# Kernel optimization log

Measured on AMD Instinct MI355X. Metric: run time of the kernel, lower is better.

## Reference

```python
import jax, jax.numpy as jnp
import numpy as np

CASCADING_LOSS = 0.85


def _bilinear_sample(img, px, py):
    """grid_sample(align_corners=True, padding_mode='zeros') in pixel coords.
    img: [B,C,H,W]; px,py: [B,H,W] absolute pixel coordinates."""
    B, C, H, W = img.shape
    x0 = jnp.floor(px)
    y0 = jnp.floor(py)
    x1 = x0 + 1.0
    y1 = y0 + 1.0
    wx1 = px - x0
    wx0 = 1.0 - wx1
    wy1 = py - y0
    wy0 = 1.0 - wy1

    def gather(yi, xi):
        valid = (xi >= 0) & (xi <= W - 1) & (yi >= 0) & (yi <= H - 1)
        xc = jnp.clip(xi, 0, W - 1).astype(jnp.int32)
        yc = jnp.clip(yi, 0, H - 1).astype(jnp.int32)
        # per-batch advanced indexing: [B,C,H,W]
        vals = jax.vmap(lambda im, yy, xx: im[:, yy, xx])(img, yc, xc)
        return vals * valid[:, None, :, :].astype(img.dtype)

    out = (gather(y0, x0) * (wy0 * wx0)[:, None, :, :]
           + gather(y0, x1) * (wy0 * wx1)[:, None, :, :]
           + gather(y1, x0) * (wy1 * wx0)[:, None, :, :]
           + gather(y1, x1) * (wy1 * wx1)[:, None, :, :])
    return out


def _add_flow(img, flw):
    # img: [B,C,H,W]; flw: [B,2,H,W] with channel 0 -> y offset, channel 1 -> x offset
    B, C, H, W = img.shape
    base_x = jnp.arange(W, dtype=img.dtype)[None, None, :]   # [1,1,W]
    base_y = jnp.arange(H, dtype=img.dtype)[None, :, None]   # [1,H,1]
    px = base_x + flw[:, 1, :, :]
    py = base_y + flw[:, 0, :, :]
    return _bilinear_sample(img, px, py)


def _compute_psnr(target, estim):
    mse = jnp.mean((target - estim) ** 2)
    return 10.0 * jnp.log(1.0 / mse) / jnp.log(jnp.asarray(10.0, target.dtype))


def setup_inputs() -> dict:
    key = jax.random.key(0)
    k1, k2, k3 = jax.random.split(key, 3)
    ITERS, B, H, W, C = 12, 4, 384, 512, 3
    flow_tup = jax.random.normal(k1, (ITERS, B, 2, H, W), dtype=jnp.float32)
    frame1 = jax.random.uniform(k2, (B, C, H, W), dtype=jnp.float32)
    frame2 = jax.random.uniform(k3, (B, C, H, W), dtype=jnp.float32)
    return {"flow_tup": flow_tup, "frame1": frame1, "frame2": frame2}


def reference(flow_tup, frame1, frame2):
    n_iters = flow_tup.shape[0]
    # vectorize warp over GRU iterations
    estims = jax.vmap(lambda f: _add_flow(frame1, f))(flow_tup)  # [I,B,C,H,W]
    psnrs = jax.vmap(lambda e: _compute_psnr(frame2, e))(estims)  # [I]
    weights = CASCADING_LOSS ** (n_iters - jnp.arange(n_iters, dtype=flow_tup.dtype))
    loss = -jnp.sum(psnrs * weights)
    return loss
```

## Files before the change

kernel.cpp:

```cpp
#include <hip/hip_runtime.h>
#include <math.h>

typedef _Float16 h2 __attribute__((ext_vector_type(2)));

static __device__ __forceinline__ h2 pkrtz(float a, float b) {
    return __builtin_bit_cast(h2, __builtin_amdgcn_cvt_pkrtz(a, b));
}

#if defined(__has_builtin)
#  if __has_builtin(__builtin_amdgcn_fdot2)
#    define HAVE_FDOT2 1
#  endif
#endif

#define ITERS 12
#define BATCH 4
#define CH 3
#define H 384
#define W 512

constexpr int HW  = H * W;
constexpr int CHW = CH * HW;
constexpr int TILE_X = 32, TILE_Y = 16;
constexpr int TX_N = W / TILE_X;
constexpr int TY_N = H / TILE_Y;
constexpr int NBLK = BATCH * TX_N * TY_N;
constexpr int HALO = 8;
constexpr int WIN_W = TILE_X + 2 * HALO;
constexpr int WROW  = WIN_W + 1;
constexpr int WIN_H = TILE_Y + 2 * HALO;
constexpr int WIN_CELLS = WROW * WIN_H;
constexpr int FSTRIDE = BATCH * 2 * HW;
constexpr int NXCD = 8;
constexpr int CHUNK = NBLK / NXCD;

__global__ __launch_bounds__(256, 6) void warp_mse_kernel(
    const float* __restrict__ flow,
    const float* __restrict__ f1,
    const float* __restrict__ f2,
    float* __restrict__ partials)
{
    __shared__ uint2 win[WIN_CELLS];

    int tid = threadIdx.x;
    int bx0 = blockIdx.x;
    int bx  = (bx0 & (NXCD - 1)) * CHUNK + (bx0 >> 3);
    int b   = bx / (TX_N * TY_N);
    int t   = bx - b * (TX_N * TY_N);
    int ty  = t / TX_N;
    int tx  = t - ty * TX_N;
    int x_t = tx * TILE_X, y_t = ty * TILE_Y;

    const float* f1b = f1 + b * CHW;
    const float* f2b = f2 + b * CHW;

    int x = x_t + 2 * (tid & 15);
    int y = y_t + (tid >> 4);
    int p = y * W + x;
    float yf = (float)y;
    const int ABASE = -((y_t - HALO) * WROW + (x_t - HALO));

    float2 tc0 = *(const float2*)(f2b + p);
    float2 tc1 = *(const float2*)(f2b + HW + p);
    float2 tc2 = *(const float2*)(f2b + 2 * HW + p);
    const float* fp = flow + b * 2 * HW + p;
    float2 fy0 = *(const float2*)(fp);
    float2 fx0 = *(const float2*)(fp + HW);
    float2 fy1 = *(const float2*)(fp + FSTRIDE);
    float2 fx1 = *(const float2*)(fp + FSTRIDE + HW);

#pragma unroll
    for (int k = 0; k < 3; ++k) {
        int q   = tid + 256 * k;
        int row = q / (WIN_W / 2);
        int cp  = q - row * (WIN_W / 2);
        int gx0 = x_t - HALO + 2 * cp;
        int gy  = y_t - HALO + row;
        int gxc = min(max(gx0, 0), W - 2);
        int gyc = min(max(gy, 0), H - 1);
        const float* src = f1b + gyc * W + gxc;
        float2 c0 = *(const float2*)(src);
        float2 c1 = *(const float2*)(src + HW);
        float2 c2 = *(const float2*)(src + 2 * HW);
        bool vy = (unsigned)gy < (unsigned)H;
        bool v0 = vy && ((unsigned)gx0 < (unsigned)W);
        bool v1 = vy && ((unsigned)(gx0 + 1) < (unsigned)W);
        if (!v0) { c0.x = 0.0f; c1.x = 0.0f; c2.x = 0.0f; }
        if (!v1) { c0.y = 0.0f; c1.y = 0.0f; c2.y = 0.0f; }
        unsigned a0 = __builtin_bit_cast(unsigned, pkrtz(c0.x, c1.x));
        unsigned b0 = __builtin_bit_cast(unsigned, pkrtz(c2.x, 0.0f));
        unsigned a1 = __builtin_bit_cast(unsigned, pkrtz(c0.y, c1.y));
        unsigned b1 = __builtin_bit_cast(unsigned, pkrtz(c2.y, 0.0f));
        int wb = row * WROW + 2 * cp;
        win[wb]     = make_uint2(a0, b0);
        win[wb + 1] = make_uint2(a1, b1);
    }
    __syncthreads();

    h2 t01[2], t2p[2];
    t01[0] = pkrtz(tc0.x, tc1.x);
    t2p[0] = pkrtz(tc2.x, 0.0f);
    t01[1] = pkrtz(tc0.y, tc1.y);
    t2p[1] = pkrtz(tc2.y, 0.0f);

    alignas(16) float acc[ITERS];
#pragma unroll
    for (int k = 0; k < ITERS; ++k) acc[k] = 0.0f;

#pragma unroll
    for (int it = 0; it < ITERS; ++it) {
        const float* fp2 = fp + 2 * FSTRIDE;
        float2 fy2 = make_float2(0.0f, 0.0f), fx2 = make_float2(0.0f, 0.0f);
        if (it + 2 < ITERS) { fy2 = *(const float2*)(fp2); fx2 = *(const float2*)(fp2 + HW); }

        float a_it = 0.0f;
#pragma unroll
        for (int j = 0; j < 2; ++j) {
            float fy = j ? fy0.y : fy0.x;
            float fx = j ? fx0.y : fx0.x;
            float pxf = (float)(x + j) + fx;
            float pyf = yf + fy;
            float x0f = floorf(pxf), y0f = floorf(pyf);
            float wx1 = pxf - x0f, wy1 = pyf - y0f;

            int a = (int)y0f * WROW + (int)x0f + ABASE;
            a = min(max(a, 0), WIN_CELLS - WROW - 2);

            uint2 c00 = win[a];
            uint2 c10 = win[a + WROW];
            uint2 c01 = win[a + 1];
            uint2 c11 = win[a + WROW + 1];

            h2 wxh = pkrtz(wx1, wx1);
            h2 wyh = pkrtz(wy1, wy1);

            h2 p00 = __builtin_bit_cast(h2, c00.x);
            h2 p01 = __builtin_bit_cast(h2, c01.x);
            h2 p10 = __builtin_bit_cast(h2, c10.x);
            h2 p11 = __builtin_bit_cast(h2, c11.x);
            h2 q00 = __builtin_bit_cast(h2, c00.y);
            h2 q01 = __builtin_bit_cast(h2, c01.y);
            h2 q10 = __builtin_bit_cast(h2, c10.y);
            h2 q11 = __builtin_bit_cast(h2, c11.y);

            h2 tA = p00 + (p01 - p00) * wxh;
            h2 bA = p10 + (p11 - p10) * wxh;
            h2 v01 = tA + (bA - tA) * wyh;
            h2 tB = q00 + (q01 - q00) * wxh;
            h2 bB = q10 + (q11 - q10) * wxh;
            h2 v2  = tB + (bB - tB) * wyh;

            h2 d01 = t01[j] - v01;
            h2 d2  = t2p[j] - v2;
#ifdef HAVE_FDOT2
            a_it = __builtin_amdgcn_fdot2(d01, d01,
                     __builtin_amdgcn_fdot2(d2, d2, a_it, false), false);
#else
            a_it += (float)d01.x * (float)d01.x + (float)d01.y * (float)d01.y
                  + (float)d2.x * (float)d2.x;
#endif
        }
        acc[it] = a_it;
        fy0 = fy1; fx0 = fx1; fy1 = fy2; fx1 = fx2; fp += FSTRIDE;
    }

    __syncthreads();
    float* scr = (float*)win;
    float4* sc4 = (float4*)scr;
    const float4* av = (const float4*)acc;
    sc4[tid * 3 + 0] = av[0];
    sc4[tid * 3 + 1] = av[1];
    sc4[tid * 3 + 2] = av[2];
    __syncthreads();

    int lane = tid & 63;
    int wv   = tid >> 6;
#pragma unroll
    for (int r = 0; r < 3; ++r) {
        int k = wv + 4 * r;
        float s = scr[lane * 12 + k]
                + scr[(lane + 64) * 12 + k]
                + scr[(lane + 128) * 12 + k]
                + scr[(lane + 192) * 12 + k];
#pragma unroll
        for (int off = 32; off > 0; off >>= 1)
            s += __shfl_down(s, off, 64);
        if (lane == 0) partials[k * NBLK + bx] = s;
    }
}

__global__ __launch_bounds__(768) void finalize_kernel(
    const float* __restrict__ partials,
    float* __restrict__ out)
{
    __shared__ float psnr_w[ITERS];
    int wave = threadIdx.x >> 6;
    int lane = threadIdx.x & 63;

    float s = 0.0f;
    const float4* pp = (const float4*)(partials + wave * NBLK);
#pragma unroll
    for (int j = 0; j < NBLK / 256; ++j) {
        float4 v = pp[lane + 64 * j];
        s += (v.x + v.y) + (v.z + v.w);
    }
#pragma unroll
    for (int off = 32; off > 0; off >>= 1)
        s += __shfl_down(s, off, 64);

    if (lane == 0) {
        float mse  = s * (1.0f / (float)(BATCH * CH * HW));
        float psnr = -10.0f * 0.30102999566398f * log2f(mse);
        float w = 1.0f;
        for (int k = 0; k < ITERS - wave; ++k) w *= 0.85f;
        psnr_w[wave] = psnr * w;
    }
    __syncthreads();
    if (threadIdx.x == 0) {
        float loss = 0.0f;
#pragma unroll
        for (int i = 0; i < ITERS; ++i) loss += psnr_w[i];
        out[0] = -loss;
    }
}

extern "C" void kernel_launch(void* const* d_in, const int* in_sizes, int n_in,
                              void* d_out, int out_size, void* d_ws, size_t ws_size,
                              hipStream_t stream) {
    const float* flow = (const float*)d_in[0];
    const float* f1   = (const float*)d_in[1];
    const float* f2   = (const float*)d_in[2];
    float* out        = (float*)d_out;
    float* partials   = (float*)d_ws;

    warp_mse_kernel<<<NBLK, 256, 0, stream>>>(flow, f1, f2, partials);
    finalize_kernel<<<1, 768, 0, stream>>>(partials, out);
}
```

Before: 127.3 us.

## Load flow as float4 per lane pair and exchange halves via shuffles

Each adjacent lane pair now loads four flow values as one float4 per lane: even lanes read the y-offset plane and odd lanes read the x-offset plane. The two lanes swap halves with __shfl_xor, so each still gets its own fy/fx pair. This replaces two float2 loads per iteration with one wider load, and the prefetch depth grows from two iterations ahead to three. The cost is extra cross-lane shuffles and selects, plus higher register pressure from the deeper float4 prefetch queue.

```diff
diff --git a/kernel.cpp b/kernel.cpp
--- a/kernel.cpp
+++ b/kernel.cpp
@@ -30,6 +30,7 @@
 constexpr int WROW  = WIN_W + 1;
 constexpr int WIN_H = TILE_Y + 2 * HALO;
 constexpr int WIN_CELLS = WROW * WIN_H;
+constexpr int PAIRS_ROW = WIN_W / 2;
 constexpr int FSTRIDE = BATCH * 2 * HW;
 constexpr int NXCD = 8;
 constexpr int CHUNK = NBLK / NXCD;
@@ -60,20 +61,23 @@
     float yf = (float)y;
     const int ABASE = -((y_t - HALO) * WROW + (x_t - HALO));
 
+    int par = tid & 1;
+    int xq  = x_t + 4 * ((tid & 15) >> 1);
+    int pq  = y * W + xq;
+
     float2 tc0 = *(const float2*)(f2b + p);
     float2 tc1 = *(const float2*)(f2b + HW + p);
     float2 tc2 = *(const float2*)(f2b + 2 * HW + p);
-    const float* fp = flow + b * 2 * HW + p;
-    float2 fy0 = *(const float2*)(fp);
-    float2 fx0 = *(const float2*)(fp + HW);
-    float2 fy1 = *(const float2*)(fp + FSTRIDE);
-    float2 fx1 = *(const float2*)(fp + FSTRIDE + HW);
+    const float* fq = flow + b * 2 * HW + pq + par * HW;
+    float4 rq0 = *(const float4*)(fq);
+    float4 rq1 = *(const float4*)(fq + FSTRIDE);
+    float4 rq2 = *(const float4*)(fq + 2 * FSTRIDE);
 
 #pragma unroll
     for (int k = 0; k < 3; ++k) {
         int q   = tid + 256 * k;
-        int row = q / (WIN_W / 2);
-        int cp  = q - row * (WIN_W / 2);
+        int row = q / PAIRS_ROW;
+        int cp  = q - row * PAIRS_ROW;
         int gx0 = x_t - HALO + 2 * cp;
         int gy  = y_t - HALO + row;
         int gxc = min(max(gx0, 0), W - 2);
@@ -109,17 +113,24 @@
 
 #pragma unroll
     for (int it = 0; it < ITERS; ++it) {
-        const float* fp2 = fp + 2 * FSTRIDE;
-        float2 fy2 = make_float2(0.0f, 0.0f), fx2 = make_float2(0.0f, 0.0f);
-        if (it + 2 < ITERS) { fy2 = *(const float2*)(fp2); fx2 = *(const float2*)(fp2 + HW); }
+        float4 rq3 = make_float4(0.f, 0.f, 0.f, 0.f);
+        if (it + 3 < ITERS) rq3 = *(const float4*)(fq + 3 * FSTRIDE);
+
+        float sel0 = par ? rq0.x : rq0.z;
+        float sel1 = par ? rq0.y : rq0.w;
+        float t0 = __shfl_xor(sel0, 1, 64);
+        float t1 = __shfl_xor(sel1, 1, 64);
+        float fyv[2], fxv[2];
+        fyv[0] = par ? t0 : rq0.x;
+        fyv[1] = par ? t1 : rq0.y;
+        fxv[0] = par ? rq0.z : t0;
+        fxv[1] = par ? rq0.w : t1;
 
         float a_it = 0.0f;
 #pragma unroll
         for (int j = 0; j < 2; ++j) {
-            float fy = j ? fy0.y : fy0.x;
-            float fx = j ? fx0.y : fx0.x;
-            float pxf = (float)(x + j) + fx;
-            float pyf = yf + fy;
+            float pxf = (float)(x + j) + fxv[j];
+            float pyf = yf + fyv[j];
             float x0f = floorf(pxf), y0f = floorf(pyf);
             float wx1 = pxf - x0f, wy1 = pyf - y0f;
 
@@ -161,7 +172,7 @@
 #endif
         }
         acc[it] = a_it;
-        fy0 = fy1; fx0 = fx1; fy1 = fy2; fx1 = fx2; fp += FSTRIDE;
+        rq0 = rq1; rq1 = rq2; rq2 = rq3; fq += FSTRIDE;
     }
 
     __syncthreads();
```

Result: no change. 128.3 us (+0.8%).
